# Kernel optimization log

Hardware: AMD Instinct MI355X
Metric: run time of the kernel (lower is better)

The kernel has to match this reference:

```python
import jax, jax.numpy as jnp
import numpy as np

B, Z, H = 2048, 512, 384
W_RESIDUAL = 0.2
N_FRAME = 32


def setup_inputs() -> dict:
    key = jax.random.key(0)
    ks = jax.random.split(key, 10)
    s = 0.02  # small-std init keeps tanh/sigmoid in a sane range
    return {
        "z": jax.random.normal(ks[0], (B, Z), jnp.float32),
        "Wih_enc": jax.random.normal(ks[1], (4 * H, Z), jnp.float32) * s,
        "Whh_enc": jax.random.normal(ks[2], (4 * H, H), jnp.float32) * s,
        "bih_enc": jnp.zeros((4 * H,), jnp.float32),
        "bhh_enc": jnp.zeros((4 * H,), jnp.float32),
        "Wih": jax.random.normal(ks[3], (4 * H, Z), jnp.float32) * s,
        "Whh": jax.random.normal(ks[4], (4 * H, H), jnp.float32) * s,
        "bih": jnp.zeros((4 * H,), jnp.float32),
        "bhh": jnp.zeros((4 * H,), jnp.float32),
        "w": jax.random.normal(ks[5], (H, Z), jnp.float32) * s,
        "b": jnp.zeros((Z,), jnp.float32),
        "fc1_w": jax.random.normal(ks[6], (Z, 2 * H), jnp.float32) * s,
        "fc1_b": jnp.zeros((Z,), jnp.float32),
        "fc2_w": jax.random.normal(ks[7], (Z, Z), jnp.float32) * s,
        "fc2_b": jnp.zeros((Z,), jnp.float32),
        "n_frame": N_FRAME,
    }


def _lstm_cell(x, h, c, Wih, Whh, bih, bhh):
    # PyTorch LSTMCell gate order: i, f, g, o
    gates = x @ Wih.T + bih + h @ Whh.T + bhh  # [B, 4H]
    i, f, g, o = jnp.split(gates, 4, axis=-1)
    c2 = jax.nn.sigmoid(f) * c + jax.nn.sigmoid(i) * jnp.tanh(g)
    h2 = jax.nn.sigmoid(o) * jnp.tanh(c2)
    return h2, c2


def reference(z, Wih_enc, Whh_enc, bih_enc, bhh_enc, Wih, Whh, bih, bhh,
              w, b, fc1_w, fc1_b, fc2_w, fc2_b, n_frame):
    Bz, Zd = z.shape
    Hd = Whh.shape[1]
    zeros = jnp.zeros((Bz, Hd), z.dtype)
    # enc_cell(z) with default zero state
    h0, c0 = _lstm_cell(z, zeros, zeros, Wih_enc, Whh_enc, bih_enc, bhh_enc)

    def step(carry, _):
        out_prev, h, c = carry
        h2, c2 = _lstm_cell(out_prev, h, c, Wih, Whh, bih, bhh)
        mul = jnp.tanh(h2 @ w + b)  # [B, Z]
        out_new = out_prev + W_RESIDUAL * mul
        return (out_new, h2, c2), (out_prev, h2, c2, out_new)

    (_, _, _), (e_seq, h_seq, c_seq, out_seq) = jax.lax.scan(
        step, (z, h0, c0), None, length=n_frame - 1)
    # seq arrays are [T-1, B, *]; original stacks along dim=1 then flattens -> [B*(T), *]
    out_full = jnp.concatenate([z[None], out_seq], axis=0)  # [T, B, Z]
    out = out_full.transpose(1, 0, 2).reshape(-1, Zd)        # [B*T, Z]
    e = e_seq.transpose(1, 0, 2).reshape(-1, Zd)             # [B*(T-1), Z]
    hh = h_seq.transpose(1, 0, 2).reshape(-1, Hd)
    cc = c_seq.transpose(1, 0, 2).reshape(-1, Hd)
    hc = jnp.concatenate([hh, cc], axis=1)                   # [B*(T-1), 2H]
    e_rec = jax.nn.relu(hc @ fc1_w.T + fc1_b) @ fc2_w.T + fc2_b
    return (out, e, e_rec)
```

## Files before the change

### kernel.cpp

```cpp
#include <hip/hip_runtime.h>
#include <hip/hip_bf16.h>
#include <math.h>

typedef unsigned short u16;
typedef __hip_bfloat16 bf16;
typedef __bf16 bf16x8 __attribute__((ext_vector_type(8)));
typedef float f32x4 __attribute__((ext_vector_type(4)));

#define B_DIM 2048
#define Z_DIM 512
#define H_DIM 384
#define G_DIM 1536
#define T_FRM 32
#define N_STEP 31
#define W_RES 0.2f
#define FC_ROWS (B_DIM * N_STEP)
#define FC_CHUNK 16384

__device__ __forceinline__ u16 f2b(float f) {
    bf16 h = __float2bfloat16(f);
    return __builtin_bit_cast(u16, h);
}
__device__ __forceinline__ float sigm(float x) { return 1.f / (1.f + __expf(-x)); }

typedef const __attribute__((address_space(1))) void* gas1_t;
typedef __attribute__((address_space(3))) void* las3_t;

__device__ __forceinline__ void gld_lds16(const void* g, void* l) {
    __builtin_amdgcn_global_load_lds((gas1_t)g, (las3_t)l, 16, 0, 0);
}


__device__ __forceinline__ void gemm64(const u16* __restrict__ A, int lda,
                                       const u16* __restrict__ B, int ldb,
                                       int arow0, int bcol0, int kch,
                                       u16* Asm, u16* Bsm, f32x4 acc[4])
{
    const int tid  = threadIdx.x;
    const int lane = tid & 63;
    const int wv   = tid >> 6;
    const int l15  = lane & 15;
    const int q    = lane >> 4;
    const int srow = tid >> 2;
    const int sk   = ((tid & 3) ^ ((tid >> 3) & 3)) * 8;
    const u16* Ab = A + (size_t)(arow0 + srow) * lda + sk;
    const u16* Bb = B + (size_t)(bcol0 + srow) * ldb + sk;
    u16* Al0 = Asm + tid * 8;
    u16* Bl0 = Bsm + tid * 8;
    const int swz  = (q ^ ((l15 >> 1) & 3)) * 8;
    const int aoff = (wv * 16 + l15) * 32 + swz;

    for (int kt = 0; kt < kch; ++kt) {
        const int ko = kt * 32;
        gld_lds16(Ab + ko, Al0);
        gld_lds16(Bb + ko, Bl0);
        __syncthreads();
        bf16x8 av = *(const bf16x8*)(Asm + aoff);
        bf16x8 bv[4];
#pragma unroll
        for (int j = 0; j < 4; ++j)
            bv[j] = *(const bf16x8*)(Bsm + (j * 16 + l15) * 32 + swz);
#pragma unroll
        for (int j = 0; j < 4; ++j)
            acc[j] = __builtin_amdgcn_mfma_f32_16x16x32_bf16(av, bv[j], acc[j], 0, 0, 0);
        __syncthreads();
    }
}

__device__ __forceinline__ void gemm_seg(const u16* __restrict__ A, int lda,
                                         const u16* __restrict__ B, int ldb,
                                         int arow0, int bcol0, int kch,
                                         u16* Asm, u16* Bsm, f32x4 acc[4][4])
{
    const int tid  = threadIdx.x;
    const int lane = tid & 63;
    const int wr   = ((tid >> 7) & 1) * 64;
    const int wc   = ((tid >> 6) & 1) * 64;
    const int l15  = lane & 15;
    const int q    = lane >> 4;
    const int srow = tid >> 2;
    const int sk   = ((tid & 3) ^ ((tid >> 3) & 3)) * 8;
    const u16* Ab = A + (size_t)(arow0 + srow) * lda + sk;
    const u16* Bb = B + (size_t)(bcol0 + srow) * ldb + sk;
    const size_t rstepA = (size_t)64 * lda;
    const size_t rstepB = (size_t)64 * ldb;
    u16* Al0 = Asm + tid * 8;
    u16* Bl0 = Bsm + tid * 8;
    const int swz = (q ^ ((l15 >> 1) & 3)) * 8;

    for (int kt = 0; kt < kch; ++kt) {
        const int ko = kt * 32;
        gld_lds16(Ab + ko,          Al0);
        gld_lds16(Ab + rstepA + ko, Al0 + 2048);
        gld_lds16(Bb + ko,          Bl0);
        gld_lds16(Bb + rstepB + ko, Bl0 + 2048);
        __syncthreads();
        bf16x8 av[4], bv[4];
#pragma unroll
        for (int i = 0; i < 4; ++i) {
            av[i] = *(const bf16x8*)(Asm + (wr + i * 16 + l15) * 32 + swz);
            bv[i] = *(const bf16x8*)(Bsm + (wc + i * 16 + l15) * 32 + swz);
        }
#pragma unroll
        for (int i = 0; i < 4; ++i)
#pragma unroll
            for (int j = 0; j < 4; ++j)
                acc[i][j] = __builtin_amdgcn_mfma_f32_16x16x32_bf16(av[i], bv[j], acc[i][j], 0, 0, 0);
        __syncthreads();
    }
}

__global__ __launch_bounds__(256, 4) void k_gates_lstm(
    const u16* __restrict__ A1, const u16* __restrict__ B1, int ld1, int k1,
    const u16* __restrict__ A2, const u16* __restrict__ B2, int lda2, int ldb2, int k2,
    const float* __restrict__ bp,
    float* __restrict__ c_fp, u16* __restrict__ h_out,
    u16* __restrict__ hcs, int s, int czero)
{
    __shared__ __attribute__((aligned(16))) u16 Asm[64 * 32];
    __shared__ __attribute__((aligned(16))) u16 Bsm[64 * 32];
    f32x4 acc[4];
    const f32x4 z4 = {0.f, 0.f, 0.f, 0.f};
#pragma unroll
    for (int j = 0; j < 4; ++j) acc[j] = z4;

    const int row0 = blockIdx.x * 64;
    const int col0 = blockIdx.y * 64;
    gemm64(A1, ld1, B1, ld1, row0, col0, k1, Asm, Bsm, acc);
    if (k2 > 0) gemm64(A2, lda2, B2, ldb2, row0, col0, k2, Asm, Bsm, acc);

    const int lane = threadIdx.x & 63;
    const int wv   = threadIdx.x >> 6;
    const int l15  = lane & 15;
    const int q4   = (lane >> 4) * 4;
    const int u    = blockIdx.y * 16 + l15;
    const float bg0 = bp[col0 + l15];
    const float bg1 = bp[col0 + 16 + l15];
    const float bg2 = bp[col0 + 32 + l15];
    const float bg3 = bp[col0 + 48 + l15];
#pragma unroll
    for (int r = 0; r < 4; ++r) {
        const int rr = row0 + wv * 16 + q4 + r;
        const size_t ci = (size_t)rr * H_DIM + u;
        const float gi = acc[0][r] + bg0;
        const float gf = acc[1][r] + bg1;
        const float gg = acc[2][r] + bg2;
        const float go = acc[3][r] + bg3;
        const float c  = czero ? 0.f : c_fp[ci];
        const float c2 = sigm(gf) * c + sigm(gi) * tanhf(gg);
        const float h2 = sigm(go) * tanhf(c2);
        c_fp[ci] = c2;
        h_out[ci] = f2b(h2);
        if (s >= 0) {
            u16* hr = hcs + ((size_t)rr * N_STEP + s) * (2 * H_DIM);
            hr[u]         = f2b(h2);
            hr[H_DIM + u] = f2b(c2);
        }
    }
}

__global__ __launch_bounds__(256, 4) void k_out(
    const u16* __restrict__ hbf, const u16* __restrict__ wT, const float* __restrict__ bias,
    float* __restrict__ out_fp, u16* __restrict__ out_bf,
    float* __restrict__ outsec, float* __restrict__ esec, int ts)
{
    __shared__ __attribute__((aligned(16))) u16 Asm[64 * 32];
    __shared__ __attribute__((aligned(16))) u16 Bsm[64 * 32];
    f32x4 acc[4];
    const f32x4 z4 = {0.f, 0.f, 0.f, 0.f};
#pragma unroll
    for (int j = 0; j < 4; ++j) acc[j] = z4;

    const int row0 = blockIdx.x * 64;
    const int col0 = blockIdx.y * 64;
    gemm64(hbf, H_DIM, wT, H_DIM, row0, col0, H_DIM / 32, Asm, Bsm, acc);

    const int lane = threadIdx.x & 63;
    const int wv   = threadIdx.x >> 6;
    const int l15  = lane & 15;
    const int q4   = (lane >> 4) * 4;
#pragma unroll
    for (int j = 0; j < 4; ++j) {
        const int col = col0 + j * 16 + l15;
        const float bv = bias[col];
#pragma unroll
        for (int r = 0; r < 4; ++r) {
            const int rr = row0 + wv * 16 + q4 + r;
            const size_t idx = (size_t)rr * Z_DIM + col;
            const float v = acc[j][r] + bv;
            const float onew = out_fp[idx] + W_RES * tanhf(v);
            out_fp[idx] = onew;
            out_bf[idx] = f2b(onew);
            outsec[((size_t)rr * T_FRM + ts) * Z_DIM + col] = onew;
            if (ts <= 30)
                esec[((size_t)rr * N_STEP + ts) * Z_DIM + col] = onew;
        }
    }
}

__global__ __launch_bounds__(256, 2) void k_fc1(
    const u16* __restrict__ A, const u16* __restrict__ B, const float* __restrict__ bias,
    u16* __restrict__ C)
{
    __shared__ __attribute__((aligned(16))) u16 Asm[128 * 32];
    __shared__ __attribute__((aligned(16))) u16 Bsm[128 * 32];
    f32x4 acc[4][4];
    const f32x4 z4 = {0.f, 0.f, 0.f, 0.f};
#pragma unroll
    for (int i = 0; i < 4; ++i)
#pragma unroll
        for (int j = 0; j < 4; ++j) acc[i][j] = z4;

    const int row0 = blockIdx.x * 128;
    const int col0 = blockIdx.y * 128;
    gemm_seg(A, 2 * H_DIM, B, 2 * H_DIM, row0, col0, 2 * H_DIM / 32, Asm, Bsm, acc);

    const int lane = threadIdx.x & 63;
    const int wr = ((threadIdx.x >> 7) & 1) * 64;
    const int wc = ((threadIdx.x >> 6) & 1) * 64;
    const int l15 = lane & 15;
    const int q4 = (lane >> 4) * 4;
#pragma unroll
    for (int j = 0; j < 4; ++j) {
        const int col = col0 + wc + j * 16 + l15;
        const float bv = bias[col];
#pragma unroll
        for (int i = 0; i < 4; ++i) {
            const int row = row0 + wr + i * 16 + q4;
#pragma unroll
            for (int r = 0; r < 4; ++r)
                C[(size_t)(row + r) * Z_DIM + col] = f2b(fmaxf(acc[i][j][r] + bv, 0.f));
        }
    }
}

__global__ __launch_bounds__(256, 2) void k_fc2(
    const u16* __restrict__ A, const u16* __restrict__ B, const float* __restrict__ bias,
    float* __restrict__ C)
{
    __shared__ __attribute__((aligned(16))) u16 Asm[128 * 32];
    __shared__ __attribute__((aligned(16))) u16 Bsm[128 * 32];
    f32x4 acc[4][4];
    const f32x4 z4 = {0.f, 0.f, 0.f, 0.f};
#pragma unroll
    for (int i = 0; i < 4; ++i)
#pragma unroll
        for (int j = 0; j < 4; ++j) acc[i][j] = z4;

    const int row0 = blockIdx.x * 128;
    const int col0 = blockIdx.y * 128;
    gemm_seg(A, Z_DIM, B, Z_DIM, row0, col0, Z_DIM / 32, Asm, Bsm, acc);

    const int lane = threadIdx.x & 63;
    const int wr = ((threadIdx.x >> 7) & 1) * 64;
    const int wc = ((threadIdx.x >> 6) & 1) * 64;
    const int l15 = lane & 15;
    const int q4 = (lane >> 4) * 4;
#pragma unroll
    for (int j = 0; j < 4; ++j) {
        const int col = col0 + wc + j * 16 + l15;
        const float bv = bias[col];
#pragma unroll
        for (int i = 0; i < 4; ++i) {
            const int row = row0 + wr + i * 16 + q4;
#pragma unroll
            for (int r = 0; r < 4; ++r)
                C[(size_t)(row + r) * Z_DIM + col] = acc[i][j][r] + bv;
        }
    }
}

__global__ void k_cvt(const float* __restrict__ src, u16* __restrict__ dst, int n)
{
    const int i = blockIdx.x * 256 + threadIdx.x;
    if (i < n) dst[i] = f2b(src[i]);
}

__global__ void k_cvtp(const float* __restrict__ src, u16* __restrict__ dst, int K)
{
    const int i = blockIdx.x * 256 + threadIdx.x;
    const int p = i / K;
    const int k = i - p * K;
    const int u = ((p >> 6) << 4) | (p & 15);
    const int g = (p >> 4) & 3;
    dst[i] = f2b(src[(size_t)(g * H_DIM + u) * K + k]);
}

__global__ void k_biasp(const float* __restrict__ b1, const float* __restrict__ b2,
                        float* __restrict__ bp)
{
    const int p = blockIdx.x * 256 + threadIdx.x;
    const int u = ((p >> 6) << 4) | (p & 15);
    const int g = (p >> 4) & 3;
    bp[p] = b1[g * H_DIM + u] + b2[g * H_DIM + u];
}

__global__ void k_init(const float* __restrict__ z, float* __restrict__ out_fp,
                       u16* __restrict__ out_bf, float* __restrict__ outsec,
                       float* __restrict__ esec)
{
    const int i = blockIdx.x * 256 + threadIdx.x;
    const int m = i >> 9;
    const int n = i & 511;
    const float zv = z[i];
    out_fp[i] = zv;
    out_bf[i] = f2b(zv);
    outsec[((size_t)m * T_FRM) * Z_DIM + n] = zv;
    esec[((size_t)m * N_STEP) * Z_DIM + n] = zv;
}

__global__ void k_trw(const float* __restrict__ w, u16* __restrict__ wT)
{
    const int i = blockIdx.x * 256 + threadIdx.x;
    const int k = i >> 9;
    const int n = i & 511;
    wT[(size_t)n * H_DIM + k] = f2b(w[i]);
}

extern "C" void kernel_launch(void* const* d_in, const int* in_sizes, int n_in,
                              void* d_out, int out_size, void* d_ws, size_t ws_size,
                              hipStream_t stream)
{
    const float* z       = (const float*)d_in[0];
    const float* Wih_enc = (const float*)d_in[1];
    const float* bih_enc = (const float*)d_in[3];
    const float* bhh_enc = (const float*)d_in[4];
    const float* Wih  = (const float*)d_in[5];
    const float* Whh  = (const float*)d_in[6];
    const float* bih  = (const float*)d_in[7];
    const float* bhh  = (const float*)d_in[8];
    const float* w    = (const float*)d_in[9];
    const float* bvec = (const float*)d_in[10];
    const float* fc1w = (const float*)d_in[11];
    const float* fc1b = (const float*)d_in[12];
    const float* fc2w = (const float*)d_in[13];
    const float* fc2b = (const float*)d_in[14];

    float* outsec = (float*)d_out;
    float* esec   = outsec + (size_t)B_DIM * T_FRM * Z_DIM;
    float* erec   = esec + (size_t)B_DIM * N_STEP * Z_DIM;

    u16* hcs_all = (u16*)((char*)erec + (size_t)FC_ROWS * 512);

    char* ws = (char*)d_ws;
    size_t off = 0;
    auto alloc = [&](size_t bytes) -> char* {
        char* p = ws + off;
        off += (bytes + 255) & ~(size_t)255;
        return p;
    };
    float* c_fp    = (float*)alloc((size_t)B_DIM * H_DIM * 4);
    float* out_fp  = (float*)alloc((size_t)B_DIM * Z_DIM * 4);
    u16*   out_bf  = (u16*)  alloc((size_t)B_DIM * Z_DIM * 2);
    u16*   hb0     = (u16*)  alloc((size_t)B_DIM * H_DIM * 2);
    u16*   hb1     = (u16*)  alloc((size_t)B_DIM * H_DIM * 2);
    u16*   wT      = (u16*)  alloc((size_t)Z_DIM * H_DIM * 2);
    u16*   t1      = (u16*)  alloc((size_t)FC_CHUNK * Z_DIM * 2);
    u16*   Wenc_bf = (u16*)  alloc((size_t)G_DIM * Z_DIM * 2);
    u16*   Wih_bf  = (u16*)  alloc((size_t)G_DIM * Z_DIM * 2);
    u16*   Whh_bf  = (u16*)  alloc((size_t)G_DIM * H_DIM * 2);
    u16*   fc1w_bf = (u16*)  alloc((size_t)Z_DIM * 2 * H_DIM * 2);
    u16*   fc2w_bf = (u16*)  alloc((size_t)Z_DIM * Z_DIM * 2);
    float* bpe     = (float*)alloc((size_t)G_DIM * 4);
    float* bpd     = (float*)alloc((size_t)G_DIM * 4);
    u16*   hbuf[2] = {hb0, hb1};

    const dim3 blk(256);
    k_cvtp<<<G_DIM * Z_DIM / 256, blk, 0, stream>>>(Wih_enc, Wenc_bf, Z_DIM);
    k_cvtp<<<G_DIM * Z_DIM / 256, blk, 0, stream>>>(Wih, Wih_bf, Z_DIM);
    k_cvtp<<<G_DIM * H_DIM / 256, blk, 0, stream>>>(Whh, Whh_bf, H_DIM);
    k_biasp<<<G_DIM / 256, blk, 0, stream>>>(bih_enc, bhh_enc, bpe);
    k_biasp<<<G_DIM / 256, blk, 0, stream>>>(bih, bhh, bpd);
    k_cvt<<<Z_DIM * 2 * H_DIM / 256, blk, 0, stream>>>(fc1w, fc1w_bf, Z_DIM * 2 * H_DIM);
    k_cvt<<<Z_DIM * Z_DIM / 256, blk, 0, stream>>>(fc2w, fc2w_bf, Z_DIM * Z_DIM);
    k_trw<<<H_DIM * Z_DIM / 256, blk, 0, stream>>>(w, wT);
    k_init<<<B_DIM * Z_DIM / 256, blk, 0, stream>>>(z, out_fp, out_bf, outsec, esec);

    k_gates_lstm<<<dim3(32, 24), blk, 0, stream>>>(
        out_bf, Wenc_bf, Z_DIM, Z_DIM / 32,
        nullptr, nullptr, 0, 0, 0,
        bpe, c_fp, hbuf[0], nullptr, -1, 1);

    for (int s = 0; s < N_STEP; ++s) {
        const u16* hp = hbuf[s & 1];
        u16*       hn = hbuf[(s + 1) & 1];
        k_gates_lstm<<<dim3(32, 24), blk, 0, stream>>>(
            out_bf, Wih_bf, Z_DIM, Z_DIM / 32,
            hp, Whh_bf, H_DIM, H_DIM, H_DIM / 32,
            bpd, c_fp, hn, hcs_all, s, 0);
        k_out<<<dim3(32, 8), blk, 0, stream>>>(hn, wT, bvec, out_fp, out_bf,
                                               outsec, esec, s + 1);
    }

    for (int r0 = 0; r0 < FC_ROWS; r0 += FC_CHUNK) {
        const int rows = (FC_ROWS - r0 < FC_CHUNK) ? (FC_ROWS - r0) : FC_CHUNK;
        k_fc1<<<dim3(rows / 128, 4), blk, 0, stream>>>(
            hcs_all + (size_t)r0 * (2 * H_DIM), fc1w_bf, fc1b, t1);
        k_fc2<<<dim3(rows / 128, 4), blk, 0, stream>>>(
            t1, fc2w_bf, fc2b, erec + (size_t)r0 * Z_DIM);
    }
}
```

Baseline: 1.447 ms.

## Double-buffer LDS tiles in all GEMM kernels and enlarge LSTM gate tile to 128 rows

Every GEMM main loop now uses two LDS buffers. The global-to-LDS load of the next K-slice is issued before computing on the current one, and the barrier count per iteration drops from two to one. The LSTM gate kernel fuses the Wih and Whh K-loops into a single pipelined loop and processes 128 rows per block instead of 64, which halves the grid to 16x24. This adds LDS and register pressure (launch bounds drop from 4 to 2 blocks per CU) and gives fewer blocks per step in the latency-bound recurrent kernels.

```diff
diff --git a/kernel.cpp b/kernel.cpp
--- a/kernel.cpp
+++ b/kernel.cpp
@@ -31,11 +31,22 @@
 }
 
 
-__device__ __forceinline__ void gemm64(const u16* __restrict__ A, int lda,
-                                       const u16* __restrict__ B, int ldb,
-                                       int arow0, int bcol0, int kch,
-                                       u16* Asm, u16* Bsm, f32x4 acc[4])
-{
+__global__ __launch_bounds__(256, 2) void k_gates_lstm(
+    const u16* __restrict__ A1, const u16* __restrict__ B1, int ld1, int k1,
+    const u16* __restrict__ A2, const u16* __restrict__ B2, int ld2, int k2,
+    const float* __restrict__ bp,
+    float* __restrict__ c_fp, u16* __restrict__ h_out,
+    u16* __restrict__ hcs, int s, int czero)
+{
+    __shared__ __attribute__((aligned(16))) u16 Asm[2][4096];
+    __shared__ __attribute__((aligned(16))) u16 Bsm[2][2048];
+    f32x4 acc[2][4];
+    const f32x4 z4 = {0.f, 0.f, 0.f, 0.f};
+#pragma unroll
+    for (int i = 0; i < 2; ++i)
+#pragma unroll
+        for (int j = 0; j < 4; ++j) acc[i][j] = z4;
+
     const int tid  = threadIdx.x;
     const int lane = tid & 63;
     const int wv   = tid >> 6;
@@ -43,142 +54,148 @@
     const int q    = lane >> 4;
     const int srow = tid >> 2;
     const int sk   = ((tid & 3) ^ ((tid >> 3) & 3)) * 8;
-    const u16* Ab = A + (size_t)(arow0 + srow) * lda + sk;
-    const u16* Bb = B + (size_t)(bcol0 + srow) * ldb + sk;
-    u16* Al0 = Asm + tid * 8;
-    u16* Bl0 = Bsm + tid * 8;
     const int swz  = (q ^ ((l15 >> 1) & 3)) * 8;
-    const int aoff = (wv * 16 + l15) * 32 + swz;
-
-    for (int kt = 0; kt < kch; ++kt) {
-        const int ko = kt * 32;
-        gld_lds16(Ab + ko, Al0);
-        gld_lds16(Bb + ko, Bl0);
+    const int row0 = blockIdx.x * 128;
+    const int col0 = blockIdx.y * 64;
+
+    const u16* A1b = A1 + (size_t)(row0 + srow) * ld1 + sk;
+    const u16* B1b = B1 + (size_t)(col0 + srow) * ld1 + sk;
+    const u16* A2b = A2 + (size_t)(row0 + srow) * ld2 + sk;
+    const u16* B2b = B2 + (size_t)(col0 + srow) * ld2 + sk;
+    u16* Ad0 = &Asm[0][0] + tid * 8;
+    u16* Bd0 = &Bsm[0][0] + tid * 8;
+    const int K = k1 + k2;
+
+    auto stage = [&](int kt, int bsel) {
+        u16* Ad = Ad0 + bsel * 4096;
+        u16* Bd = Bd0 + bsel * 2048;
+        if (kt < k1) {
+            const u16* Ap = A1b + kt * 32;
+            gld_lds16(Ap, Ad);
+            gld_lds16(Ap + (size_t)64 * ld1, Ad + 2048);
+            gld_lds16(B1b + kt * 32, Bd);
+        } else {
+            const u16* Ap = A2b + (kt - k1) * 32;
+            gld_lds16(Ap, Ad);
+            gld_lds16(Ap + (size_t)64 * ld2, Ad + 2048);
+            gld_lds16(B2b + (kt - k1) * 32, Bd);
+        }
+    };
+    auto compute = [&](int bsel) {
+        const u16* As = &Asm[bsel][0];
+        const u16* Bs = &Bsm[bsel][0];
+        bf16x8 av[2], bv[4];
+#pragma unroll
+        for (int i = 0; i < 2; ++i)
+            av[i] = *(const bf16x8*)(As + (wv * 32 + i * 16 + l15) * 32 + swz);
+#pragma unroll
+        for (int j = 0; j < 4; ++j)
+            bv[j] = *(const bf16x8*)(Bs + (j * 16 + l15) * 32 + swz);
+#pragma unroll
+        for (int i = 0; i < 2; ++i)
+#pragma unroll
+            for (int j = 0; j < 4; ++j)
+                acc[i][j] = __builtin_amdgcn_mfma_f32_16x16x32_bf16(av[i], bv[j], acc[i][j], 0, 0, 0);
+    };
+
+    stage(0, 0);
+    __syncthreads();
+    int cur = 0;
+    for (int kt = 0; kt < K - 1; ++kt) {
+        stage(kt + 1, cur ^ 1);
+        compute(cur);
         __syncthreads();
-        bf16x8 av = *(const bf16x8*)(Asm + aoff);
-        bf16x8 bv[4];
-#pragma unroll
-        for (int j = 0; j < 4; ++j)
-            bv[j] = *(const bf16x8*)(Bsm + (j * 16 + l15) * 32 + swz);
-#pragma unroll
-        for (int j = 0; j < 4; ++j)
-            acc[j] = __builtin_amdgcn_mfma_f32_16x16x32_bf16(av, bv[j], acc[j], 0, 0, 0);
-        __syncthreads();
-    }
-}
-
-__device__ __forceinline__ void gemm_seg(const u16* __restrict__ A, int lda,
-                                         const u16* __restrict__ B, int ldb,
-                                         int arow0, int bcol0, int kch,
-                                         u16* Asm, u16* Bsm, f32x4 acc[4][4])
-{
+        cur ^= 1;
+    }
+    compute(cur);
+
+    const int q4 = q * 4;
+    const int u  = blockIdx.y * 16 + l15;
+    const float bg0 = bp[col0 + l15];
+    const float bg1 = bp[col0 + 16 + l15];
+    const float bg2 = bp[col0 + 32 + l15];
+    const float bg3 = bp[col0 + 48 + l15];
+#pragma unroll
+    for (int i = 0; i < 2; ++i) {
+#pragma unroll
+        for (int r = 0; r < 4; ++r) {
+            const int rr = row0 + wv * 32 + i * 16 + q4 + r;
+            const size_t ci = (size_t)rr * H_DIM + u;
+            const float gi = acc[i][0][r] + bg0;
+            const float gf = acc[i][1][r] + bg1;
+            const float gg = acc[i][2][r] + bg2;
+            const float go = acc[i][3][r] + bg3;
+            const float c  = czero ? 0.f : c_fp[ci];
+            const float c2 = sigm(gf) * c + sigm(gi) * tanhf(gg);
+            const float h2 = sigm(go) * tanhf(c2);
+            c_fp[ci] = c2;
+            h_out[ci] = f2b(h2);
+            if (s >= 0) {
+                u16* hr = hcs + ((size_t)rr * N_STEP + s) * (2 * H_DIM);
+                hr[u]         = f2b(h2);
+                hr[H_DIM + u] = f2b(c2);
+            }
+        }
+    }
+}
+
+__global__ __launch_bounds__(256, 2) void k_out(
+    const u16* __restrict__ hbf, const u16* __restrict__ wT, const float* __restrict__ bias,
+    float* __restrict__ out_fp, u16* __restrict__ out_bf,
+    float* __restrict__ outsec, float* __restrict__ esec, int ts)
+{
+    __shared__ __attribute__((aligned(16))) u16 Asm[2][2048];
+    __shared__ __attribute__((aligned(16))) u16 Bsm[2][2048];
+    f32x4 acc[4];
+    const f32x4 z4 = {0.f, 0.f, 0.f, 0.f};
+#pragma unroll
+    for (int j = 0; j < 4; ++j) acc[j] = z4;
+
     const int tid  = threadIdx.x;
     const int lane = tid & 63;
-    const int wr   = ((tid >> 7) & 1) * 64;
-    const int wc   = ((tid >> 6) & 1) * 64;
+    const int wv   = tid >> 6;
     const int l15  = lane & 15;
     const int q    = lane >> 4;
     const int srow = tid >> 2;
     const int sk   = ((tid & 3) ^ ((tid >> 3) & 3)) * 8;
-    const u16* Ab = A + (size_t)(arow0 + srow) * lda + sk;
-    const u16* Bb = B + (size_t)(bcol0 + srow) * ldb + sk;
-    const size_t rstepA = (size_t)64 * lda;
-    const size_t rstepB = (size_t)64 * ldb;
-    u16* Al0 = Asm + tid * 8;
-    u16* Bl0 = Bsm + tid * 8;
-    const int swz = (q ^ ((l15 >> 1) & 3)) * 8;
-
-    for (int kt = 0; kt < kch; ++kt) {
-        const int ko = kt * 32;
-        gld_lds16(Ab + ko,          Al0);
-        gld_lds16(Ab + rstepA + ko, Al0 + 2048);
-        gld_lds16(Bb + ko,          Bl0);
-        gld_lds16(Bb + rstepB + ko, Bl0 + 2048);
-        __syncthreads();
-        bf16x8 av[4], bv[4];
-#pragma unroll
-        for (int i = 0; i < 4; ++i) {
-            av[i] = *(const bf16x8*)(Asm + (wr + i * 16 + l15) * 32 + swz);
-            bv[i] = *(const bf16x8*)(Bsm + (wc + i * 16 + l15) * 32 + swz);
-        }
-#pragma unroll
-        for (int i = 0; i < 4; ++i)
-#pragma unroll
-            for (int j = 0; j < 4; ++j)
-                acc[i][j] = __builtin_amdgcn_mfma_f32_16x16x32_bf16(av[i], bv[j], acc[i][j], 0, 0, 0);
-        __syncthreads();
-    }
-}
-
-__global__ __launch_bounds__(256, 4) void k_gates_lstm(
-    const u16* __restrict__ A1, const u16* __restrict__ B1, int ld1, int k1,
-    const u16* __restrict__ A2, const u16* __restrict__ B2, int lda2, int ldb2, int k2,
-    const float* __restrict__ bp,
-    float* __restrict__ c_fp, u16* __restrict__ h_out,
-    u16* __restrict__ hcs, int s, int czero)
-{
-    __shared__ __attribute__((aligned(16))) u16 Asm[64 * 32];
-    __shared__ __attribute__((aligned(16))) u16 Bsm[64 * 32];
-    f32x4 acc[4];
-    const f32x4 z4 = {0.f, 0.f, 0.f, 0.f};
-#pragma unroll
-    for (int j = 0; j < 4; ++j) acc[j] = z4;
-
+    const int swz  = (q ^ ((l15 >> 1) & 3)) * 8;
     const int row0 = blockIdx.x * 64;
     const int col0 = blockIdx.y * 64;
-    gemm64(A1, ld1, B1, ld1, row0, col0, k1, Asm, Bsm, acc);
-    if (k2 > 0) gemm64(A2, lda2, B2, ldb2, row0, col0, k2, Asm, Bsm, acc);
-
-    const int lane = threadIdx.x & 63;
-    const int wv   = threadIdx.x >> 6;
-    const int l15  = lane & 15;
-    const int q4   = (lane >> 4) * 4;
-    const int u    = blockIdx.y * 16 + l15;
-    const float bg0 = bp[col0 + l15];
-    const float bg1 = bp[col0 + 16 + l15];
-    const float bg2 = bp[col0 + 32 + l15];
-    const float bg3 = bp[col0 + 48 + l15];
-#pragma unroll
-    for (int r = 0; r < 4; ++r) {
-        const int rr = row0 + wv * 16 + q4 + r;
-        const size_t ci = (size_t)rr * H_DIM + u;
-        const float gi = acc[0][r] + bg0;
-        const float gf = acc[1][r] + bg1;
-        const float gg = acc[2][r] + bg2;
-        const float go = acc[3][r] + bg3;
-        const float c  = czero ? 0.f : c_fp[ci];
-        const float c2 = sigm(gf) * c + sigm(gi) * tanhf(gg);
-        const float h2 = sigm(go) * tanhf(c2);
-        c_fp[ci] = c2;
-        h_out[ci] = f2b(h2);
-        if (s >= 0) {
-            u16* hr = hcs + ((size_t)rr * N_STEP + s) * (2 * H_DIM);
-            hr[u]         = f2b(h2);
-            hr[H_DIM + u] = f2b(c2);
-        }
-    }
-}
-
-__global__ __launch_bounds__(256, 4) void k_out(
-    const u16* __restrict__ hbf, const u16* __restrict__ wT, const float* __restrict__ bias,
-    float* __restrict__ out_fp, u16* __restrict__ out_bf,
-    float* __restrict__ outsec, float* __restrict__ esec, int ts)
-{
-    __shared__ __attribute__((aligned(16))) u16 Asm[64 * 32];
-    __shared__ __attribute__((aligned(16))) u16 Bsm[64 * 32];
-    f32x4 acc[4];
-    const f32x4 z4 = {0.f, 0.f, 0.f, 0.f};
-#pragma unroll
-    for (int j = 0; j < 4; ++j) acc[j] = z4;
-
-    const int row0 = blockIdx.x * 64;
-    const int col0 = blockIdx.y * 64;
-    gemm64(hbf, H_DIM, wT, H_DIM, row0, col0, H_DIM / 32, Asm, Bsm, acc);
-
-    const int lane = threadIdx.x & 63;
-    const int wv   = threadIdx.x >> 6;
-    const int l15  = lane & 15;
-    const int q4   = (lane >> 4) * 4;
+    const u16* Ab = hbf + (size_t)(row0 + srow) * H_DIM + sk;
+    const u16* Bb = wT  + (size_t)(col0 + srow) * H_DIM + sk;
+    u16* Ad0 = &Asm[0][0] + tid * 8;
+    u16* Bd0 = &Bsm[0][0] + tid * 8;
+    const int aoff = (wv * 16 + l15) * 32 + swz;
+
+    auto stage = [&](int kt, int bsel) {
+        gld_lds16(Ab + kt * 32, Ad0 + bsel * 2048);
+        gld_lds16(Bb + kt * 32, Bd0 + bsel * 2048);
+    };
+    auto compute = [&](int bsel) {
+        const u16* As = &Asm[bsel][0];
+        const u16* Bs = &Bsm[bsel][0];
+        bf16x8 av = *(const bf16x8*)(As + aoff);
+        bf16x8 bv[4];
+#pragma unroll
+        for (int j = 0; j < 4; ++j)
+            bv[j] = *(const bf16x8*)(Bs + (j * 16 + l15) * 32 + swz);
+#pragma unroll
+        for (int j = 0; j < 4; ++j)
+            acc[j] = __builtin_amdgcn_mfma_f32_16x16x32_bf16(av, bv[j], acc[j], 0, 0, 0);
+    };
+
+    stage(0, 0);
+    __syncthreads();
+    int cur = 0;
+    for (int kt = 0; kt < H_DIM / 32 - 1; ++kt) {
+        stage(kt + 1, cur ^ 1);
+        compute(cur);
+        __syncthreads();
+        cur ^= 1;
+    }
+    compute(cur);
+
+    const int q4 = q * 4;
 #pragma unroll
     for (int j = 0; j < 4; ++j) {
         const int col = col0 + j * 16 + l15;
@@ -198,12 +215,71 @@
     }
 }
 
+__device__ __forceinline__ void gemm128_pipe(const u16* __restrict__ A, int lda,
+                                             const u16* __restrict__ B, int ldb,
+                                             int arow0, int bcol0, int kch,
+                                             u16 (*Asm)[4096], u16 (*Bsm)[4096],
+                                             f32x4 acc[4][4])
+{
+    const int tid  = threadIdx.x;
+    const int lane = tid & 63;
+    const int wr   = ((tid >> 7) & 1) * 64;
+    const int wc   = ((tid >> 6) & 1) * 64;
+    const int l15  = lane & 15;
+    const int q    = lane >> 4;
+    const int srow = tid >> 2;
+    const int sk   = ((tid & 3) ^ ((tid >> 3) & 3)) * 8;
+    const int swz  = (q ^ ((l15 >> 1) & 3)) * 8;
+    const u16* Ab = A + (size_t)(arow0 + srow) * lda + sk;
+    const u16* Bb = B + (size_t)(bcol0 + srow) * ldb + sk;
+    const size_t rstepA = (size_t)64 * lda;
+    const size_t rstepB = (size_t)64 * ldb;
+    u16* Ad0 = &Asm[0][0] + tid * 8;
+    u16* Bd0 = &Bsm[0][0] + tid * 8;
+
+    auto stage = [&](int kt, int bsel) {
+        const int ko = kt * 32;
+        u16* Ad = Ad0 + bsel * 4096;
+        u16* Bd = Bd0 + bsel * 4096;
+        gld_lds16(Ab + ko,          Ad);
+        gld_lds16(Ab + rstepA + ko, Ad + 2048);
+        gld_lds16(Bb + ko,          Bd);
+        gld_lds16(Bb + rstepB + ko, Bd + 2048);
+    };
+    auto compute = [&](int bsel) {
+        const u16* As = &Asm[bsel][0];
+        const u16* Bs = &Bsm[bsel][0];
+        bf16x8 av[4], bv[4];
+#pragma unroll
+        for (int i = 0; i < 4; ++i) {
+            av[i] = *(const bf16x8*)(As + (wr + i * 16 + l15) * 32 + swz);
+            bv[i] = *(const bf16x8*)(Bs + (wc + i * 16 + l15) * 32 + swz);
+        }
+#pragma unroll
+        for (int i = 0; i < 4; ++i)
+#pragma unroll
+            for (int j = 0; j < 4; ++j)
+                acc[i][j] = __builtin_amdgcn_mfma_f32_16x16x32_bf16(av[i], bv[j], acc[i][j], 0, 0, 0);
+    };
+
+    stage(0, 0);
+    __syncthreads();
+    int cur = 0;
+    for (int kt = 0; kt < kch - 1; ++kt) {
+        stage(kt + 1, cur ^ 1);
+        compute(cur);
+        __syncthreads();
+        cur ^= 1;
+    }
+    compute(cur);
+}
+
 __global__ __launch_bounds__(256, 2) void k_fc1(
     const u16* __restrict__ A, const u16* __restrict__ B, const float* __restrict__ bias,
     u16* __restrict__ C)
 {
-    __shared__ __attribute__((aligned(16))) u16 Asm[128 * 32];
-    __shared__ __attribute__((aligned(16))) u16 Bsm[128 * 32];
+    __shared__ __attribute__((aligned(16))) u16 Asm[2][4096];
+    __shared__ __attribute__((aligned(16))) u16 Bsm[2][4096];
     f32x4 acc[4][4];
     const f32x4 z4 = {0.f, 0.f, 0.f, 0.f};
 #pragma unroll
@@ -213,7 +289,7 @@
 
     const int row0 = blockIdx.x * 128;
     const int col0 = blockIdx.y * 128;
-    gemm_seg(A, 2 * H_DIM, B, 2 * H_DIM, row0, col0, 2 * H_DIM / 32, Asm, Bsm, acc);
+    gemm128_pipe(A, 2 * H_DIM, B, 2 * H_DIM, row0, col0, 2 * H_DIM / 32, Asm, Bsm, acc);
 
     const int lane = threadIdx.x & 63;
     const int wr = ((threadIdx.x >> 7) & 1) * 64;
@@ -238,8 +314,8 @@
     const u16* __restrict__ A, const u16* __restrict__ B, const float* __restrict__ bias,
     float* __restrict__ C)
 {
-    __shared__ __attribute__((aligned(16))) u16 Asm[128 * 32];
-    __shared__ __attribute__((aligned(16))) u16 Bsm[128 * 32];
+    __shared__ __attribute__((aligned(16))) u16 Asm[2][4096];
+    __shared__ __attribute__((aligned(16))) u16 Bsm[2][4096];
     f32x4 acc[4][4];
     const f32x4 z4 = {0.f, 0.f, 0.f, 0.f};
 #pragma unroll
@@ -249,7 +325,7 @@
 
     const int row0 = blockIdx.x * 128;
     const int col0 = blockIdx.y * 128;
-    gemm_seg(A, Z_DIM, B, Z_DIM, row0, col0, Z_DIM / 32, Asm, Bsm, acc);
+    gemm128_pipe(A, Z_DIM, B, Z_DIM, row0, col0, Z_DIM / 32, Asm, Bsm, acc);
 
     const int lane = threadIdx.x & 63;
     const int wr = ((threadIdx.x >> 7) & 1) * 64;
@@ -265,7 +341,7 @@
             const int row = row0 + wr + i * 16 + q4;
 #pragma unroll
             for (int r = 0; r < 4; ++r)
-                C[(size_t)(row + r) * Z_DIM + col] = acc[i][j][r] + bv;
+                C[(size_t)(row + r) * (Z_DIM) + col] = acc[i][j][r] + bv;
         }
     }
 }
@@ -376,17 +452,17 @@
     k_trw<<<H_DIM * Z_DIM / 256, blk, 0, stream>>>(w, wT);
     k_init<<<B_DIM * Z_DIM / 256, blk, 0, stream>>>(z, out_fp, out_bf, outsec, esec);
 
-    k_gates_lstm<<<dim3(32, 24), blk, 0, stream>>>(
+    k_gates_lstm<<<dim3(16, 24), blk, 0, stream>>>(
         out_bf, Wenc_bf, Z_DIM, Z_DIM / 32,
-        nullptr, nullptr, 0, 0, 0,
+        out_bf, Wenc_bf, Z_DIM, 0,
         bpe, c_fp, hbuf[0], nullptr, -1, 1);
 
     for (int s = 0; s < N_STEP; ++s) {
         const u16* hp = hbuf[s & 1];
         u16*       hn = hbuf[(s + 1) & 1];
-        k_gates_lstm<<<dim3(32, 24), blk, 0, stream>>>(
+        k_gates_lstm<<<dim3(16, 24), blk, 0, stream>>>(
             out_bf, Wih_bf, Z_DIM, Z_DIM / 32,
-            hp, Whh_bf, H_DIM, H_DIM, H_DIM / 32,
+            hp, Whh_bf, H_DIM, H_DIM / 32,
             bpd, c_fp, hn, hcs_all, s, 0);
         k_out<<<dim3(32, 8), blk, 0, stream>>>(hn, wT, bvec, out_fp, out_bf,
                                                outsec, esec, s + 1);
```

Measured after the change: 1.574 ms. 1.09x slower.
